# Kernel optimization log

Measured on AMD Instinct MI355X. Metric: run time of the kernel, lower is better.

The kernel has to match this reference:

```python
import jax, jax.numpy as jnp
import numpy as np

N_NODES = 100000
N_EDGES = 1600000
N_GRAPHS = 128
D = 64
EPS = 1e-5


def layer_norm(h, gamma, beta):
    mu = jnp.mean(h, axis=-1, keepdims=True)
    var = jnp.var(h, axis=-1, keepdims=True)
    return (h - mu) * jax.lax.rsqrt(var + EPS) * gamma + beta


def setup_inputs() -> dict:
    key = jax.random.key(0)
    ks = jax.random.split(key, 9)
    x = jax.random.normal(ks[0], (N_NODES, D), dtype=jnp.float32)
    edge_index = jax.random.randint(ks[1], (2, N_EDGES), 0, N_NODES, dtype=jnp.int64)
    batch = jnp.sort(jax.random.randint(ks[2], (N_NODES,), 0, N_GRAPHS, dtype=jnp.int64))
    graph_embed = jax.random.normal(ks[3], (N_GRAPHS, D), dtype=jnp.float32)
    s = 1.0 / np.sqrt(D)
    W_self = jax.random.uniform(ks[4], (D, D), jnp.float32, -s, s)
    W_neigh = jax.random.uniform(ks[5], (D, D), jnp.float32, -s, s)
    b = jax.random.uniform(ks[6], (D,), jnp.float32, -s, s)
    gamma = jnp.ones((D,), jnp.float32)
    beta = jnp.zeros((D,), jnp.float32)
    return {"x": x, "edge_index": edge_index, "batch": batch,
            "graph_embed": graph_embed, "W_self": W_self, "W_neigh": W_neigh,
            "b": b, "gamma": gamma, "beta": beta}


def reference(x, edge_index, batch, graph_embed, W_self, W_neigh, b, gamma, beta):
    src, dst = edge_index[0], edge_index[1]
    # mean neighbor aggregation: gather src features, scatter-add into dst
    msg_sum = jax.ops.segment_sum(x[src], dst, num_segments=N_NODES)  # [N, D]
    deg = jax.ops.segment_sum(jnp.ones((N_EDGES,), x.dtype), dst, num_segments=N_NODES)
    h_neigh = msg_sum / jnp.maximum(deg, 1.0)[:, None]
    # SAGEConv combine
    node_out = x @ W_self + h_neigh @ W_neigh + b  # [N, D]
    # graph_aggr='add' pooling over batch assignment
    graph_out = jax.ops.segment_sum(node_out, batch, num_segments=N_GRAPHS)  # [G, D]
    # residual (channel_match=True -> no projection)
    node_out = node_out + x
    graph_out = graph_out + graph_embed
    # norm then act; note: original applies norm TWICE to graph_out and no ReLU on it
    node_out = jax.nn.relu(layer_norm(node_out, gamma, beta))
    graph_out = layer_norm(layer_norm(graph_out, gamma, beta), gamma, beta)
    return (node_out, graph_out)
```

## Files before the change

kernel.cpp:

```cpp
#include <hip/hip_runtime.h>

#define N_NODES  100000
#define N_EDGES  1600000
#define N_GRAPHS 128
#define DD       64
#define EPSV     1e-5f

#define BSH      5
#define BMASK    31
#define NBUCK    3125
#define CAPB     768

#define THRP     1024
#define EPT      16
#define BLKE     (THRP*EPT)
#define NBLK     ((N_EDGES + BLKE - 1) / BLKE)

#define O_CUR   0u
#define O_BKT   200704u
#define O_GACC  9801216u
#define O_XB    9834496u
#define O_WTF   22634496u
#define WS_NEED (O_WTF + 16384u)

typedef __attribute__((ext_vector_type(8))) short bf16x8;
typedef __attribute__((ext_vector_type(4))) float f32x4;
typedef __attribute__((ext_vector_type(2))) float f32x2;

__device__ __forceinline__ ushort bf16rne(float f) {
  uint u = __float_as_uint(f);
  return (ushort)((u + 0x7FFFu + ((u >> 16) & 1u)) >> 16);
}
__device__ __forceinline__ uint pk2(float lo, float hi) {
  return (uint)bf16rne(lo) | ((uint)bf16rne(hi) << 16);
}

__global__ __launch_bounds__(256) void cast_k(const float* __restrict__ x, ushort* __restrict__ xb,
                                              int* __restrict__ cur, float* __restrict__ gacc) {
  int i = blockIdx.x * 256 + threadIdx.x;
  if (i < NBUCK * 16) cur[i] = 0;
  if (i < N_GRAPHS * DD) gacc[i] = 0.f;
  if (i < 128) gacc[N_GRAPHS * DD + i] = 0.f;
  float4 v = ((const float4*)x)[i];
  uint4 u = *(const uint4*)&v;
  ushort4 o;
  o.x = (ushort)((u.x + 0x7FFFu + ((u.x >> 16) & 1)) >> 16);
  o.y = (ushort)((u.y + 0x7FFFu + ((u.y >> 16) & 1)) >> 16);
  o.z = (ushort)((u.z + 0x7FFFu + ((u.z >> 16) & 1)) >> 16);
  o.w = (ushort)((u.w + 0x7FFFu + ((u.w >> 16) & 1)) >> 16);
  ((ushort4*)xb)[i] = o;
}

__global__ __launch_bounds__(1024) void scatP_k(const int* __restrict__ ei, int* __restrict__ cur,
                                                int* __restrict__ bkt,
                                                const float* __restrict__ Wself,
                                                const float* __restrict__ Wneigh,
                                                ushort* __restrict__ wtf) {
  __shared__ int hist[NBUCK];
  int t = threadIdx.x;
  if (blockIdx.x == 0) {
    int lane = t & 63, ks = (t >> 6) & 3, tile = (t >> 8) & 1, nt = t >> 9;
    int brow = (nt << 5) + (tile << 4) + (lane & 15);
    int k0 = (ks << 5) + (((lane >> 4) & 3) << 3);
    uint4 o;
    uint p[4];
#pragma unroll
    for (int jj = 0; jj < 4; ++jj) {
      int k = k0 + jj * 2;
      float w0 = (k < 64)     ? Wself[k * DD + brow]       : Wneigh[(k - 64) * DD + brow];
      float w1 = (k + 1 < 64) ? Wself[(k + 1) * DD + brow] : Wneigh[(k - 63) * DD + brow];
      p[jj] = pk2(w0, w1);
    }
    o.x = p[0]; o.y = p[1]; o.z = p[2]; o.w = p[3];
    ((uint4*)wtf)[t] = o;
  }
  for (int i = t; i < NBUCK; i += THRP) hist[i] = 0;
  __syncthreads();
  int e0 = blockIdx.x * BLKE;
  int pk[EPT], bn[EPT];
#pragma unroll
  for (int j = 0; j < EPT; ++j) {
    int e = e0 + j * THRP + t;
    bn[j] = -1;
    if (e < N_EDGES) {
      int s = ei[e], d = ei[N_EDGES + e];
      bn[j] = d >> BSH;
      pk[j] = s | ((d & BMASK) << 17);
      atomicAdd(&hist[bn[j]], 1);
    }
  }
  __syncthreads();
  for (int b = t; b < NBUCK; b += THRP) {
    int c = hist[b];
    hist[b] = c ? atomicAdd(&cur[b * 16], c) : 0;
  }
  __syncthreads();
#pragma unroll
  for (int j = 0; j < EPT; ++j) {
    if (bn[j] >= 0) {
      int sp = atomicAdd(&hist[bn[j]], 1);
      if (sp < CAPB) bkt[bn[j] * CAPB + sp] = pk[j];
    }
  }
}

__global__ __launch_bounds__(256, 8) void aggM_k(const ushort* __restrict__ xb,
                                                 const int* __restrict__ cur,
                                                 const int* __restrict__ bkt,
                                                 const ushort* __restrict__ wtf,
                                                 const float* __restrict__ bvec,
                                                 const float* __restrict__ gamma,
                                                 const float* __restrict__ beta,
                                                 const int* __restrict__ batch,
                                                 float* __restrict__ gacc,
                                                 float* __restrict__ out) {
  __shared__ short As[32 * 128];
  __shared__ float Cbuf[32 * 65];
  __shared__ int sorted[CAPB + 16];
  __shared__ int hist[32], startc[32], curl[32];
  int t = threadIdx.x;
  int b = blockIdx.x;
  int node0 = b << BSH;
  if (t < 32) hist[t] = 0;
  {
    uint4 v = ((const uint4*)(xb + (size_t)node0 * DD))[t];
    uint r = (uint)t >> 3, c = (uint)t & 7;
    *(uint4*)((char*)As + r * 256u + ((c * 16u) ^ ((r & 7u) << 4))) = v;
  }
  __syncthreads();
  int n = cur[b * 16];
  if (n > CAPB) n = CAPB;
  int boff = b * CAPB;
  int w0 = -1, w1 = -1, w2 = -1;
  if (t < n)       { w0 = bkt[boff + t];       atomicAdd(&hist[w0 >> 17], 1); }
  if (t + 256 < n) { w1 = bkt[boff + t + 256]; atomicAdd(&hist[w1 >> 17], 1); }
  if (t + 512 < n) { w2 = bkt[boff + t + 512]; atomicAdd(&hist[w2 >> 17], 1); }
  __syncthreads();
  if (t < 32) {
    int h = hist[t];
    int v = h;
#pragma unroll
    for (int off = 1; off < 32; off <<= 1) {
      int u = __shfl_up(v, off);
      if (t >= off) v += u;
    }
    startc[t] = v - h;
    curl[t]   = v - h;
  }
  __syncthreads();
  if (w0 >= 0) { int p = atomicAdd(&curl[w0 >> 17], 1); sorted[p] = ((w0 & 0x1FFFF) << 7) + 512; }
  if (w1 >= 0) { int p = atomicAdd(&curl[w1 >> 17], 1); sorted[p] = ((w1 & 0x1FFFF) << 7) + 512; }
  if (w2 >= 0) { int p = atomicAdd(&curl[w2 >> 17], 1); sorted[p] = ((w2 & 0x1FFFF) << 7) + 512; }
  __syncthreads();
  int wl   = __builtin_amdgcn_readfirstlane(t >> 6);
  int lane = t & 63;
  int g    = lane >> 4;
  int sub  = lane & 15;
  const char* zb = (const char*)xb - 512;
  uint subb = (uint)sub * 8u;
  for (int r = wl; r < 32; r += 4) {
    int s0 = startc[r], dg = hist[r];
    f32x2 A01 = {0.f, 0.f}, A23 = {0.f, 0.f};
    for (int j = 0; j < dg; j += 16) {
      int e0 = j + g, e1 = j + 4 + g, e2 = j + 8 + g, e3 = j + 12 + g;
      uint o0 = (uint)sorted[s0 + e0]; if (e0 >= dg) o0 = 0u;
      uint o1 = (uint)sorted[s0 + e1]; if (e1 >= dg) o1 = 0u;
      uint o2 = (uint)sorted[s0 + e2]; if (e2 >= dg) o2 = 0u;
      uint o3 = (uint)sorted[s0 + e3]; if (e3 >= dg) o3 = 0u;
      uint2 u0 = *(const uint2*)(zb + o0 + subb);
      uint2 u1 = *(const uint2*)(zb + o1 + subb);
      uint2 u2 = *(const uint2*)(zb + o2 + subb);
      uint2 u3 = *(const uint2*)(zb + o3 + subb);
      f32x2 v0, v1, v2, v3, y0, y1, y2, y3;
      v0.x = __uint_as_float(u0.x << 16); v0.y = __uint_as_float(u0.x & 0xFFFF0000u);
      v1.x = __uint_as_float(u1.x << 16); v1.y = __uint_as_float(u1.x & 0xFFFF0000u);
      v2.x = __uint_as_float(u2.x << 16); v2.y = __uint_as_float(u2.x & 0xFFFF0000u);
      v3.x = __uint_as_float(u3.x << 16); v3.y = __uint_as_float(u3.x & 0xFFFF0000u);
      y0.x = __uint_as_float(u0.y << 16); y0.y = __uint_as_float(u0.y & 0xFFFF0000u);
      y1.x = __uint_as_float(u1.y << 16); y1.y = __uint_as_float(u1.y & 0xFFFF0000u);
      y2.x = __uint_as_float(u2.y << 16); y2.y = __uint_as_float(u2.y & 0xFFFF0000u);
      y3.x = __uint_as_float(u3.y << 16); y3.y = __uint_as_float(u3.y & 0xFFFF0000u);
      A01 += (v0 + v1) + (v2 + v3);
      A23 += (y0 + y1) + (y2 + y3);
    }
    float a0 = A01.x, a1 = A01.y, a2 = A23.x, a3 = A23.y;
#pragma unroll
    for (int off = 16; off <= 32; off <<= 1) {
      a0 += __shfl_xor(a0, off);
      a1 += __shfl_xor(a1, off);
      a2 += __shfl_xor(a2, off);
      a3 += __shfl_xor(a3, off);
    }
    if (g == 0) {
      float inv = 1.f / fmaxf((float)dg, 1.f);
      uint2 pw;
      pw.x = pk2(a0 * inv, a1 * inv);
      pw.y = pk2(a2 * inv, a3 * inv);
      uint rr = (uint)r;
      *(uint2*)((char*)As + rr * 256u + ((128u + (uint)sub * 8u) ^ ((rr & 7u) << 4))) = pw;
    }
  }
  __syncthreads();
  f32x4 acc0 = {0.f, 0.f, 0.f, 0.f}, acc1 = {0.f, 0.f, 0.f, 0.f};
  uint mrow  = (uint)(wl >> 1) << 4;
  int  nt    = wl & 1;
  uint arow  = mrow + (uint)(lane & 15);
  uint kc    = ((uint)(lane >> 4)) * 16u;
#pragma unroll 1
  for (int ks = 0; ks < 4; ++ks) {
    uint kb = (uint)ks * 64u + kc;
    bf16x8 af = *(const bf16x8*)((const char*)As + arow * 256u + (kb ^ ((arow & 7u) << 4)));
    bf16x8 b0 = *(const bf16x8*)(wtf + (size_t)(((nt * 2 + 0) * 4 + ks) * 64 + lane) * 8);
    bf16x8 b1 = *(const bf16x8*)(wtf + (size_t)(((nt * 2 + 1) * 4 + ks) * 64 + lane) * 8);
    acc0 = __builtin_amdgcn_mfma_f32_16x16x32_bf16(af, b0, acc0, 0, 0, 0);
    acc1 = __builtin_amdgcn_mfma_f32_16x16x32_bf16(af, b1, acc1, 0, 0, 0);
  }
  {
    uint nbase = (uint)nt << 5;
    uint rr = mrow + (((uint)(lane >> 4)) << 2);
    uint cc = nbase + (uint)(lane & 15);
#pragma unroll
    for (int j = 0; j < 4; ++j) {
      uint rj = rr + (uint)j;
      Cbuf[rj * 65u + cc]       = acc0[j];
      Cbuf[rj * 65u + cc + 16u] = acc1[j];
    }
  }
  __syncthreads();
  float bv  = bvec[lane];
  float gv  = gamma[lane];
  float btv = beta[lane];
  int r0 = wl * 8;
  int gprev = -1; float pool = 0.f;
#pragma unroll
  for (int m = 0; m < 8; ++m) {
    uint r = (uint)(r0 + m);
    int node = node0 + r0 + m;
    float cval = Cbuf[r * 65u + (uint)lane];
    float tmp = cval + bv;
    int gi = batch[node];
    if (gi != gprev) {
      if (gprev >= 0) atomicAdd(&gacc[gprev * DD + lane], pool);
      pool = 0.f; gprev = gi;
    }
    pool += tmp;
    ushort xv16 = *(const ushort*)((const char*)As + r * 256u + (((uint)lane * 2u) ^ ((r & 7u) << 4)));
    float val = tmp + __uint_as_float((uint)xv16 << 16);
    float s = val;
    for (int off = 32; off; off >>= 1) s += __shfl_xor(s, off);
    float mu  = s * (1.f / 64.f);
    float dlt = val - mu;
    float ss  = dlt * dlt;
    for (int off = 32; off; off >>= 1) ss += __shfl_xor(ss, off);
    float rstd = rsqrtf(ss * (1.f / 64.f) + EPSV);
    float o = dlt * rstd * gv + btv;
    out[(size_t)node * DD + lane] = fmaxf(o, 0.f);
  }
  if (gprev >= 0) atomicAdd(&gacc[gprev * DD + lane], pool);
}

__global__ __launch_bounds__(256) void graph_k(const float* __restrict__ gacc, const float* __restrict__ gemb,
                                               const float* __restrict__ gamma, const float* __restrict__ beta,
                                               float* __restrict__ out) {
  int lane = threadIdx.x & 63;
  int w = blockIdx.x * 4 + (threadIdx.x >> 6);
  if (w >= N_GRAPHS) return;
  float v = gacc[w * DD + lane] + gemb[w * DD + lane];
  float gv = gamma[lane], btv = beta[lane];
#pragma unroll
  for (int it = 0; it < 2; ++it) {
    float s = v;
    for (int off = 32; off; off >>= 1) s += __shfl_xor(s, off);
    float mu  = s * (1.f / 64.f);
    float d   = v - mu;
    float ss  = d * d;
    for (int off = 32; off; off >>= 1) ss += __shfl_xor(ss, off);
    v = d * rsqrtf(ss * (1.f / 64.f) + EPSV) * gv + btv;
  }
  out[(size_t)N_NODES * DD + w * DD + lane] = v;
}

extern "C" void kernel_launch(void* const* d_in, const int* in_sizes, int n_in,
                              void* d_out, int out_size, void* d_ws, size_t ws_size,
                              hipStream_t stream) {
  const float* x      = (const float*)d_in[0];
  const int*   ei     = (const int*)d_in[1];
  const int*   batch  = (const int*)d_in[2];
  const float* gemb   = (const float*)d_in[3];
  const float* Wself  = (const float*)d_in[4];
  const float* Wneigh = (const float*)d_in[5];
  const float* bvec   = (const float*)d_in[6];
  const float* gamma  = (const float*)d_in[7];
  const float* beta   = (const float*)d_in[8];

  char* ws = (char*)d_ws;
  int*    cur  = (int*)(ws + O_CUR);
  int*    bkt  = (int*)(ws + O_BKT);
  float*  gacc = (float*)(ws + O_GACC);
  ushort* xb   = (ushort*)(ws + O_XB);
  ushort* wtf  = (ushort*)(ws + O_WTF);
  float*  outf = (float*)d_out;

  cast_k <<<N_NODES * DD / 4 / 256, 256, 0, stream>>>(x, xb, cur, gacc);
  scatP_k<<<NBLK, THRP, 0, stream>>>(ei, cur, bkt, Wself, Wneigh, wtf);
  aggM_k <<<NBUCK, 256, 0, stream>>>(xb, cur, bkt, wtf, bvec, gamma, beta,
                                     batch, gacc, outf);
  graph_k<<<N_GRAPHS / 4, 256, 0, stream>>>(gacc, gemb, gamma, beta, outf);
}
```

Before: 92.82 us.

## Replace global atomic bucketing with per-block local sort and descriptor gather

```diff
diff --git a/kernel.cpp b/kernel.cpp
--- a/kernel.cpp
+++ b/kernel.cpp
@@ -9,6 +9,7 @@
 #define BSH      5
 #define BMASK    31
 #define NBUCK    3125
+#define NBPAD    4096
 #define CAPB     768
 
 #define THRP     1024
@@ -16,8 +17,8 @@
 #define BLKE     (THRP*EPT)
 #define NBLK     ((N_EDGES + BLKE - 1) / BLKE)
 
-#define O_CUR   0u
-#define O_BKT   200704u
+#define O_ORD   200704u
+#define O_DESC  6754304u
 #define O_GACC  9801216u
 #define O_XB    9834496u
 #define O_WTF   22634496u
@@ -36,9 +37,8 @@
 }
 
 __global__ __launch_bounds__(256) void cast_k(const float* __restrict__ x, ushort* __restrict__ xb,
-                                              int* __restrict__ cur, float* __restrict__ gacc) {
+                                              float* __restrict__ gacc) {
   int i = blockIdx.x * 256 + threadIdx.x;
-  if (i < NBUCK * 16) cur[i] = 0;
   if (i < N_GRAPHS * DD) gacc[i] = 0.f;
   if (i < 128) gacc[N_GRAPHS * DD + i] = 0.f;
   float4 v = ((const float4*)x)[i];
@@ -51,12 +51,15 @@
   ((ushort4*)xb)[i] = o;
 }
 
-__global__ __launch_bounds__(1024) void scatP_k(const int* __restrict__ ei, int* __restrict__ cur,
-                                                int* __restrict__ bkt,
+__global__ __launch_bounds__(1024) void scatS_k(const int* __restrict__ ei,
+                                                int* __restrict__ ordered,
+                                                int* __restrict__ desc,
                                                 const float* __restrict__ Wself,
                                                 const float* __restrict__ Wneigh,
                                                 ushort* __restrict__ wtf) {
-  __shared__ int hist[NBUCK];
+  __shared__ int hist[NBPAD];
+  __shared__ int cur2[NBPAD];
+  __shared__ int wtot[16];
   int t = threadIdx.x;
   if (blockIdx.x == 0) {
     int lane = t & 63, ks = (t >> 6) & 3, tile = (t >> 8) & 1, nt = t >> 9;
@@ -74,7 +77,7 @@
     o.x = p[0]; o.y = p[1]; o.z = p[2]; o.w = p[3];
     ((uint4*)wtf)[t] = o;
   }
-  for (int i = t; i < NBUCK; i += THRP) hist[i] = 0;
+  for (int i = t; i < NBPAD; i += THRP) hist[i] = 0;
   __syncthreads();
   int e0 = blockIdx.x * BLKE;
   int pk[EPT], bn[EPT];
@@ -90,23 +93,55 @@
     }
   }
   __syncthreads();
-  for (int b = t; b < NBUCK; b += THRP) {
-    int c = hist[b];
-    hist[b] = c ? atomicAdd(&cur[b * 16], c) : 0;
-  }
-  __syncthreads();
+  int h0 = hist[4 * t], h1 = hist[4 * t + 1], h2 = hist[4 * t + 2], h3 = hist[4 * t + 3];
+  int s = h0 + h1 + h2 + h3;
+  int lane = t & 63, wv = t >> 6;
+  int inc = s;
+#pragma unroll
+  for (int off = 1; off < 64; off <<= 1) {
+    int u = __shfl_up(inc, off);
+    if (lane >= off) inc += u;
+  }
+  if (lane == 63) wtot[wv] = inc;
+  __syncthreads();
+  if (t < 16) {
+    int v = wtot[t];
+    int iv = v;
+#pragma unroll
+    for (int off = 1; off < 16; off <<= 1) {
+      int u = __shfl_up(iv, off);
+      if (t >= off) iv += u;
+    }
+    wtot[t] = iv - v;
+  }
+  __syncthreads();
+  int base = wtot[wv] + (inc - s);
+  cur2[4 * t]     = base;
+  cur2[4 * t + 1] = base + h0;
+  cur2[4 * t + 2] = base + h0 + h1;
+  cur2[4 * t + 3] = base + h0 + h1 + h2;
+  {
+    int dbase = blockIdx.x * NBUCK;
+#pragma unroll
+    for (int i = 0; i < 4; ++i) {
+      int bb = 4 * t + i;
+      if (bb < NBUCK) desc[dbase + bb] = (cur2[bb] << 10) | hist[bb];
+    }
+  }
+  __syncthreads();
+  int obase = blockIdx.x * BLKE;
 #pragma unroll
   for (int j = 0; j < EPT; ++j) {
     if (bn[j] >= 0) {
-      int sp = atomicAdd(&hist[bn[j]], 1);
-      if (sp < CAPB) bkt[bn[j] * CAPB + sp] = pk[j];
+      int sp = atomicAdd(&cur2[bn[j]], 1);
+      ordered[obase + sp] = pk[j];
     }
   }
 }
 
 __global__ __launch_bounds__(256, 8) void aggM_k(const ushort* __restrict__ xb,
-                                                 const int* __restrict__ cur,
-                                                 const int* __restrict__ bkt,
+                                                 const int* __restrict__ ordered,
+                                                 const int* __restrict__ desc,
                                                  const ushort* __restrict__ wtf,
                                                  const float* __restrict__ bvec,
                                                  const float* __restrict__ gamma,
@@ -118,6 +153,9 @@
   __shared__ float Cbuf[32 * 65];
   __shared__ int sorted[CAPB + 16];
   __shared__ int hist[32], startc[32], curl[32];
+  __shared__ int wsum2[2];
+  __shared__ int nTot_s;
+  int* slabL = (int*)Cbuf;
   int t = threadIdx.x;
   int b = blockIdx.x;
   int node0 = b << BSH;
@@ -127,14 +165,36 @@
     uint r = (uint)t >> 3, c = (uint)t & 7;
     *(uint4*)((char*)As + r * 256u + ((c * 16u) ^ ((r & 7u) << 4))) = v;
   }
-  __syncthreads();
-  int n = cur[b * 16];
+  int dsc = (t < NBLK) ? desc[t * NBUCK + b] : 0;
+  int c   = dsc & 1023;
+  int st  = dsc >> 10;
+  int inc = c;
+  if (t < 128) {
+    int lane = t & 63;
+#pragma unroll
+    for (int off = 1; off < 64; off <<= 1) {
+      int u = __shfl_up(inc, off);
+      if (lane >= off) inc += u;
+    }
+    if (lane == 63) wsum2[t >> 6] = inc;
+  }
+  __syncthreads();
+  int pos = 0;
+  if (t < 128) pos = ((t >> 6) ? wsum2[0] : 0) + inc - c;
+  if (t == 0) nTot_s = wsum2[0] + wsum2[1];
+  if (t < NBLK) {
+    int lim = CAPB - pos;
+    int cc = c < lim ? c : (lim > 0 ? lim : 0);
+    const int* srcp = ordered + (size_t)t * BLKE + st;
+    for (int i = 0; i < cc; ++i) slabL[pos + i] = srcp[i];
+  }
+  __syncthreads();
+  int n = nTot_s;
   if (n > CAPB) n = CAPB;
-  int boff = b * CAPB;
   int w0 = -1, w1 = -1, w2 = -1;
-  if (t < n)       { w0 = bkt[boff + t];       atomicAdd(&hist[w0 >> 17], 1); }
-  if (t + 256 < n) { w1 = bkt[boff + t + 256]; atomicAdd(&hist[w1 >> 17], 1); }
-  if (t + 512 < n) { w2 = bkt[boff + t + 512]; atomicAdd(&hist[w2 >> 17], 1); }
+  if (t < n)       { w0 = slabL[t];       atomicAdd(&hist[w0 >> 17], 1); }
+  if (t + 256 < n) { w1 = slabL[t + 256]; atomicAdd(&hist[w1 >> 17], 1); }
+  if (t + 512 < n) { w2 = slabL[t + 512]; atomicAdd(&hist[w2 >> 17], 1); }
   __syncthreads();
   if (t < 32) {
     int h = hist[t];
@@ -294,16 +354,16 @@
   const float* beta   = (const float*)d_in[8];
 
   char* ws = (char*)d_ws;
-  int*    cur  = (int*)(ws + O_CUR);
-  int*    bkt  = (int*)(ws + O_BKT);
-  float*  gacc = (float*)(ws + O_GACC);
-  ushort* xb   = (ushort*)(ws + O_XB);
-  ushort* wtf  = (ushort*)(ws + O_WTF);
-  float*  outf = (float*)d_out;
-
-  cast_k <<<N_NODES * DD / 4 / 256, 256, 0, stream>>>(x, xb, cur, gacc);
-  scatP_k<<<NBLK, THRP, 0, stream>>>(ei, cur, bkt, Wself, Wneigh, wtf);
-  aggM_k <<<NBUCK, 256, 0, stream>>>(xb, cur, bkt, wtf, bvec, gamma, beta,
+  int*    ordered = (int*)(ws + O_ORD);
+  int*    desc    = (int*)(ws + O_DESC);
+  float*  gacc    = (float*)(ws + O_GACC);
+  ushort* xb      = (ushort*)(ws + O_XB);
+  ushort* wtf     = (ushort*)(ws + O_WTF);
+  float*  outf    = (float*)d_out;
+
+  cast_k <<<N_NODES * DD / 4 / 256, 256, 0, stream>>>(x, xb, gacc);
+  scatS_k<<<NBLK, THRP, 0, stream>>>(ei, ordered, desc, Wself, Wneigh, wtf);
+  aggM_k <<<NBUCK, 256, 0, stream>>>(xb, ordered, desc, wtf, bvec, gamma, beta,
                                      batch, gacc, outf);
   graph_k<<<N_GRAPHS / 4, 256, 0, stream>>>(gacc, gemb, gamma, beta, outf);
 }
```

Result: faster. 89.40 us (-3.7%).
